# Kernel tuning notes

Measured on AMD Instinct MI355X. Metric: run time of the kernel, lower is better.

The kernel has to match this reference:

```python
import jax, jax.numpy as jnp
import numpy as np

B, C, L = 8192, 1, 4096
SCALES = 5
OUT_DIM = 512
STD_FACTOR = 1.0
SQRT_HALF = 0.7071067811865476  # Haar filter coefficient 1/sqrt(2)


def setup_inputs() -> dict:
    key = jax.random.key(0)
    k1, k2 = jax.random.split(key)
    x = jax.random.normal(k1, (B, C, L), dtype=jnp.float32)
    # kaiming_uniform_(a=0): bound = sqrt(2) * sqrt(3 / fan_in)
    fan_in = L  # in_dim_wave == in_dim for dyadic Haar
    bound = np.sqrt(2.0) * np.sqrt(3.0 / fan_in)
    block_mat = jax.random.uniform(k2, (L, OUT_DIM), dtype=jnp.float32,
                                   minval=-bound, maxval=bound)
    return {"x": x, "block_mat": block_mat}


def haar_analysis(x, scales):
    """Multi-level Haar DWT over last axis. Returns [cA_n, cD_n, ..., cD_1]."""
    details = []
    cur = x
    for _ in range(scales):
        even, odd = cur[..., ::2], cur[..., 1::2]
        details.append((even - odd) * SQRT_HALF)  # highpass
        cur = (even + odd) * SQRT_HALF            # lowpass
    return [cur] + details[::-1]


def reference(x, block_mat):
    coeffs = haar_analysis(x, SCALES)
    x_freq_cat = jnp.concatenate(coeffs, axis=-1)        # [B, C, L]
    c_no = x_freq_cat.shape[-1]
    x_freq_mat = x_freq_cat.reshape(-1, c_no)            # [B*C, L]
    a = jnp.abs(x_freq_mat)
    # torch.std is unbiased (ddof=1)
    threshold = jnp.mean(a) + jnp.std(a, ddof=1) * STD_FACTOR
    mask = a > threshold
    # sparse.mm(sparse(masked x), W) == (x * mask) @ W
    x_sparse = jnp.where(mask, x_freq_mat, jnp.zeros((), x_freq_mat.dtype))
    out = jax.nn.relu(x_sparse @ block_mat)              # [B*C, OUT_DIM]
    return out.reshape(x_freq_cat.shape[:-1] + (OUT_DIM,))
```

## Files before the change

kernel.cpp:

```cpp
#include <hip/hip_runtime.h>
#include <hip/hip_bf16.h>
#include <math.h>

#define LDIM 4096
#define NROWS 8192
#define NOUT 512

static const float SQRT_HALF_F = 0.70710678118654752440f;

typedef __attribute__((ext_vector_type(8))) short short8;
typedef __attribute__((ext_vector_type(4))) float f32x4;
typedef __attribute__((ext_vector_type(8))) unsigned short u16x8;
typedef __attribute__((ext_vector_type(4))) unsigned short u16x4;
typedef __attribute__((ext_vector_type(2))) unsigned short u16x2;

#define AM_OFF   0ull
#define WT_OFF   67108864ull
#define PART_OFF (WT_OFF + 4194304ull)
#define THR_OFF  (PART_OFF + 131072ull)

__device__ inline unsigned short f2bf(float f) {
  union { float f; unsigned u; } v; v.f = f;
  unsigned r = (v.u + 0x7fffu + ((v.u >> 16) & 1u)) >> 16;
  return (unsigned short)r;
}

__device__ inline unsigned short mcvt(float f, float thr) {
  return f2bf((fabsf(f) > thr) ? f : 0.0f);
}

__device__ inline void async16(void* l, const void* g) {
  __builtin_amdgcn_global_load_lds((const __attribute__((address_space(1))) void*)g,
                                   (__attribute__((address_space(3))) void*)l, 16, 0, 0);
}

__global__ __launch_bounds__(256) void haar1_kernel(const float* __restrict__ x,
                                                    double* __restrict__ partials,
                                                    const float* __restrict__ W,
                                                    unsigned short* __restrict__ Wt) {
  if (blockIdx.x >= NROWS) {
    __shared__ float tile[32][33];
    const int wb = blockIdx.x - NROWS;
    const int bx = wb & 15;
    const int by = wb >> 4;
    const int tx = threadIdx.x & 31, ty = threadIdx.x >> 5;
#pragma unroll
    for (int j = 0; j < 4; ++j)
      tile[ty + j * 8][tx] = W[(size_t)(by * 32 + ty + j * 8) * NOUT + bx * 32 + tx];
    __syncthreads();
#pragma unroll
    for (int j = 0; j < 4; ++j)
      Wt[(size_t)(bx * 32 + ty + j * 8) * LDIM + by * 32 + tx] = f2bf(tile[tx][ty + j * 8]);
    return;
  }

  __shared__ double red[8];
  const int row = blockIdx.x;
  const int t = threadIdx.x;
  const float S = SQRT_HALF_F;

  const float4* xr = (const float4*)(x + (size_t)row * LDIM) + 4 * t;
  float v[16];
#pragma unroll
  for (int k = 0; k < 4; ++k) {
    float4 q = xr[k];
    v[4 * k] = q.x; v[4 * k + 1] = q.y; v[4 * k + 2] = q.z; v[4 * k + 3] = q.w;
  }

  double sa = 0.0, sq = 0.0;
  float a1[8], a2[4], a3[2], a4;
#pragma unroll
  for (int j = 0; j < 8; ++j) {
    float d = (v[2 * j] - v[2 * j + 1]) * S;
    a1[j] = (v[2 * j] + v[2 * j + 1]) * S;
    sa += (double)fabsf(d); sq += (double)d * (double)d;
  }
#pragma unroll
  for (int j = 0; j < 4; ++j) {
    float d = (a1[2 * j] - a1[2 * j + 1]) * S;
    a2[j] = (a1[2 * j] + a1[2 * j + 1]) * S;
    sa += (double)fabsf(d); sq += (double)d * (double)d;
  }
#pragma unroll
  for (int j = 0; j < 2; ++j) {
    float d = (a2[2 * j] - a2[2 * j + 1]) * S;
    a3[j] = (a2[2 * j] + a2[2 * j + 1]) * S;
    sa += (double)fabsf(d); sq += (double)d * (double)d;
  }
  {
    float d = (a3[0] - a3[1]) * S;
    a4 = (a3[0] + a3[1]) * S;
    sa += (double)fabsf(d); sq += (double)d * (double)d;
  }
  {
    float other = __shfl_xor(a4, 1, 64);
    if ((t & 1) == 0) {
      float d = (a4 - other) * S, ap = (a4 + other) * S;
      sa += (double)fabsf(d) + (double)fabsf(ap);
      sq += (double)d * (double)d + (double)ap * (double)ap;
    }
  }

  const int lane = t & 63, wid = t >> 6;
#pragma unroll
  for (int off = 32; off > 0; off >>= 1) {
    sa += __shfl_down(sa, off, 64);
    sq += __shfl_down(sq, off, 64);
  }
  if (lane == 0) { red[wid] = sa; red[4 + wid] = sq; }
  __syncthreads();
  if (t == 0) {
    partials[2 * (size_t)row + 0] = red[0] + red[1] + red[2] + red[3];
    partials[2 * (size_t)row + 1] = red[4] + red[5] + red[6] + red[7];
  }
}

__global__ __launch_bounds__(1024) void thr_kernel(const double* __restrict__ partials,
                                                   float* __restrict__ thr) {
  __shared__ double red[32];
  const int tid = threadIdx.x;
  double sa = 0.0, sq = 0.0;
#pragma unroll
  for (int k = 0; k < NROWS / 1024; ++k) {
    int i = tid + k * 1024;
    sa += partials[2 * i + 0];
    sq += partials[2 * i + 1];
  }
  const int lane = tid & 63, wid = tid >> 6;
#pragma unroll
  for (int off = 32; off > 0; off >>= 1) {
    sa += __shfl_down(sa, off, 64);
    sq += __shfl_down(sq, off, 64);
  }
  if (lane == 0) { red[wid] = sa; red[16 + wid] = sq; }
  __syncthreads();
  if (tid == 0) {
    double s = 0.0, q = 0.0;
#pragma unroll
    for (int i = 0; i < 16; ++i) { s += red[i]; q += red[16 + i]; }
    const double n = (double)NROWS * (double)LDIM;
    double mean = s / n;
    double var = (q - s * s / n) / (n - 1.0);
    *thr = (float)(mean + sqrt(var));
  }
}

__global__ __launch_bounds__(256) void haar2_kernel(const float* __restrict__ x,
                                                    const float* __restrict__ thrp,
                                                    unsigned short* __restrict__ Am) {
  const float thr = *thrp;
  const int row = blockIdx.x;
  const int t = threadIdx.x;
  const float S = SQRT_HALF_F;

  const float4* xr = (const float4*)(x + (size_t)row * LDIM) + 4 * t;
  float v[16];
#pragma unroll
  for (int k = 0; k < 4; ++k) {
    float4 q = xr[k];
    v[4 * k] = q.x; v[4 * k + 1] = q.y; v[4 * k + 2] = q.z; v[4 * k + 3] = q.w;
  }

  unsigned short* orow = Am + (size_t)row * LDIM;
  float a1[8], a2[4], a3[2], a4;

  u16x8 d1;
#pragma unroll
  for (int j = 0; j < 8; ++j) {
    float d = (v[2 * j] - v[2 * j + 1]) * S;
    a1[j] = (v[2 * j] + v[2 * j + 1]) * S;
    d1[j] = mcvt(d, thr);
  }
  *(u16x8*)(orow + 2048 + 8 * t) = d1;

  u16x4 d2;
#pragma unroll
  for (int j = 0; j < 4; ++j) {
    float d = (a1[2 * j] - a1[2 * j + 1]) * S;
    a2[j] = (a1[2 * j] + a1[2 * j + 1]) * S;
    d2[j] = mcvt(d, thr);
  }
  *(u16x4*)(orow + 1024 + 4 * t) = d2;

  u16x2 d3;
#pragma unroll
  for (int j = 0; j < 2; ++j) {
    float d = (a2[2 * j] - a2[2 * j + 1]) * S;
    a3[j] = (a2[2 * j] + a2[2 * j + 1]) * S;
    d3[j] = mcvt(d, thr);
  }
  *(u16x2*)(orow + 512 + 2 * t) = d3;

  {
    float d = (a3[0] - a3[1]) * S;
    a4 = (a3[0] + a3[1]) * S;
    orow[256 + t] = mcvt(d, thr);
  }
  {
    float other = __shfl_xor(a4, 1, 64);
    if ((t & 1) == 0) {
      float d = (a4 - other) * S, ap = (a4 + other) * S;
      orow[128 + t / 2] = mcvt(d, thr);
      orow[t / 2] = mcvt(ap, thr);
    }
  }
}

__global__ __launch_bounds__(512) void gemm_kernel(const unsigned short* __restrict__ Am,
                                                   const unsigned short* __restrict__ Wt,
                                                   float* __restrict__ out) {
  __shared__ __align__(16) unsigned short As[128 * 64];
  __shared__ __align__(16) unsigned short Bs[64 * 64];

  const int tid = threadIdx.x;
  const int lane = tid & 63, w = tid >> 6;
  const int quad = lane >> 4, l15 = lane & 15;
  const int wm = w >> 1, wn = w & 1;

  const int id = blockIdx.x;
  const int xcd = id & 7, slot = id >> 3;
  const int nblk = slot & 7;
  const int mblk = (slot >> 3) * 8 + xcd;
  const int n0 = nblk * 64, m0 = mblk * 128;

  f32x4 acc[2][2] = {};

  const int rl = lane >> 3;
  const int cg = (lane & 7) ^ rl;
  const unsigned short* AgBase = Am + (size_t)(m0 + rl) * LDIM + cg * 8;
  const unsigned short* BgBase = Wt + (size_t)(n0 + rl) * LDIM + cg * 8;

  for (int k0 = 0; k0 < LDIM; k0 += 64) {
#pragma unroll
    for (int j = 0; j < 2; ++j)
      async16(&As[(w * 2 + j) * 512], AgBase + (size_t)((w * 2 + j) * 8) * LDIM + k0);
    async16(&Bs[w * 512], BgBase + (size_t)(w * 8) * LDIM + k0);
    __syncthreads();

    short8 af[2][2], bf[2][2];
#pragma unroll
    for (int mi = 0; mi < 2; ++mi) {
      const int row = wm * 32 + mi * 16 + l15;
#pragma unroll
      for (int ks = 0; ks < 2; ++ks)
        af[mi][ks] = *(const short8*)&As[row * 64 + ((ks * 4 + quad) ^ (row & 7)) * 8];
    }
#pragma unroll
    for (int ni = 0; ni < 2; ++ni) {
      const int row = wn * 32 + ni * 16 + l15;
#pragma unroll
      for (int ks = 0; ks < 2; ++ks)
        bf[ni][ks] = *(const short8*)&Bs[row * 64 + ((ks * 4 + quad) ^ (row & 7)) * 8];
    }
#pragma unroll
    for (int ks = 0; ks < 2; ++ks)
#pragma unroll
      for (int mi = 0; mi < 2; ++mi)
#pragma unroll
        for (int ni = 0; ni < 2; ++ni)
          acc[mi][ni] = __builtin_amdgcn_mfma_f32_16x16x32_bf16(af[mi][ks], bf[ni][ks],
                                                                acc[mi][ni], 0, 0, 0);
    __syncthreads();
  }

#pragma unroll
  for (int mi = 0; mi < 2; ++mi) {
#pragma unroll
    for (int ni = 0; ni < 2; ++ni) {
      const int r0 = m0 + wm * 32 + mi * 16 + quad * 4;
      const int c = n0 + wn * 32 + ni * 16 + l15;
#pragma unroll
      for (int r = 0; r < 4; ++r)
        out[(size_t)(r0 + r) * NOUT + c] = fmaxf(acc[mi][ni][r], 0.0f);
    }
  }
}

extern "C" void kernel_launch(void* const* d_in, const int* in_sizes, int n_in,
                              void* d_out, int out_size, void* d_ws, size_t ws_size,
                              hipStream_t stream) {
  const float* x = (const float*)d_in[0];
  const float* W = (const float*)d_in[1];
  float* out = (float*)d_out;

  char* ws = (char*)d_ws;
  unsigned short* Am = (unsigned short*)(ws + AM_OFF);
  unsigned short* Wt = (unsigned short*)(ws + WT_OFF);
  double* partials = (double*)(ws + PART_OFF);
  float* thr = (float*)(ws + THR_OFF);

  haar1_kernel<<<NROWS + 2048, 256, 0, stream>>>(x, partials, W, Wt);
  thr_kernel<<<1, 1024, 0, stream>>>(partials, thr);
  haar2_kernel<<<NROWS, 256, 0, stream>>>(x, thr, Am);
  gemm_kernel<<<512, 512, 0, stream>>>(Am, Wt, out);
}
```

Measured before the change: 268.0 us.

## Restructure GEMM as intra-block split-K with per-wave double-buffered async loads

The GEMM now uses 64x64 output tiles with 256-thread blocks, where each of the four waves owns a separate quarter of the K dimension. Each wave stages its slices into private LDS double buffers via async loads, waiting on vmcnt instead of block-wide barriers. The per-wave partial sums are reduced through LDS at the end, then ReLU is applied and stores are vectorized. This removes per-iteration __syncthreads and overlaps loads with MFMA, at the cost of extra LDS reduction traffic and lower tile reuse from the smaller M tile.

Result: slower. 286.5 us (+6.9%).

```diff
diff --git a/kernel.cpp b/kernel.cpp
--- a/kernel.cpp
+++ b/kernel.cpp
@@ -206,73 +206,99 @@
   }
 }
 
-__global__ __launch_bounds__(512) void gemm_kernel(const unsigned short* __restrict__ Am,
-                                                   const unsigned short* __restrict__ Wt,
-                                                   float* __restrict__ out) {
-  __shared__ __align__(16) unsigned short As[128 * 64];
-  __shared__ __align__(16) unsigned short Bs[64 * 64];
+__global__ __launch_bounds__(256, 2) void gemm_kernel(const unsigned short* __restrict__ Am,
+                                                      const unsigned short* __restrict__ Wt,
+                                                      float* __restrict__ out) {
+  __shared__ __align__(16) unsigned short lds[4 * 2 * 4096];
 
   const int tid = threadIdx.x;
   const int lane = tid & 63, w = tid >> 6;
   const int quad = lane >> 4, l15 = lane & 15;
-  const int wm = w >> 1, wn = w & 1;
 
   const int id = blockIdx.x;
   const int xcd = id & 7, slot = id >> 3;
   const int nblk = slot & 7;
   const int mblk = (slot >> 3) * 8 + xcd;
-  const int n0 = nblk * 64, m0 = mblk * 128;
-
-  f32x4 acc[2][2] = {};
-
-  const int rl = lane >> 3;
-  const int cg = (lane & 7) ^ rl;
-  const unsigned short* AgBase = Am + (size_t)(m0 + rl) * LDIM + cg * 8;
-  const unsigned short* BgBase = Wt + (size_t)(n0 + rl) * LDIM + cg * 8;
-
-  for (int k0 = 0; k0 < LDIM; k0 += 64) {
-#pragma unroll
-    for (int j = 0; j < 2; ++j)
-      async16(&As[(w * 2 + j) * 512], AgBase + (size_t)((w * 2 + j) * 8) * LDIM + k0);
-    async16(&Bs[w * 512], BgBase + (size_t)(w * 8) * LDIM + k0);
-    __syncthreads();
-
-    short8 af[2][2], bf[2][2];
-#pragma unroll
-    for (int mi = 0; mi < 2; ++mi) {
-      const int row = wm * 32 + mi * 16 + l15;
-#pragma unroll
-      for (int ks = 0; ks < 2; ++ks)
-        af[mi][ks] = *(const short8*)&As[row * 64 + ((ks * 4 + quad) ^ (row & 7)) * 8];
-    }
-#pragma unroll
-    for (int ni = 0; ni < 2; ++ni) {
-      const int row = wn * 32 + ni * 16 + l15;
-#pragma unroll
-      for (int ks = 0; ks < 2; ++ks)
-        bf[ni][ks] = *(const short8*)&Bs[row * 64 + ((ks * 4 + quad) ^ (row & 7)) * 8];
-    }
-#pragma unroll
-    for (int ks = 0; ks < 2; ++ks)
-#pragma unroll
-      for (int mi = 0; mi < 2; ++mi)
-#pragma unroll
-        for (int ni = 0; ni < 2; ++ni)
-          acc[mi][ni] = __builtin_amdgcn_mfma_f32_16x16x32_bf16(af[mi][ks], bf[ni][ks],
-                                                                acc[mi][ni], 0, 0, 0);
-    __syncthreads();
-  }
-
-#pragma unroll
-  for (int mi = 0; mi < 2; ++mi) {
-#pragma unroll
-    for (int ni = 0; ni < 2; ++ni) {
-      const int r0 = m0 + wm * 32 + mi * 16 + quad * 4;
-      const int c = n0 + wn * 32 + ni * 16 + l15;
-#pragma unroll
-      for (int r = 0; r < 4; ++r)
-        out[(size_t)(r0 + r) * NOUT + c] = fmaxf(acc[mi][ni][r], 0.0f);
-    }
+  const int n0 = nblk * 64, m0 = mblk * 64;
+
+  f32x4 acc[4][4] = {};
+
+  const int r = lane >> 2, p = lane & 3;
+  const int c = p ^ ((r >> 1) & 3);
+  const int kw = w * 32;
+  const unsigned short* Ag = Am + (size_t)(m0 + r) * LDIM + kw + c * 8;
+  const unsigned short* Bg = Wt + (size_t)(n0 + r) * LDIM + kw + c * 8;
+
+  unsigned short* wbase = &lds[w * 8192];
+
+  const int sw = (quad ^ ((l15 >> 1) & 3)) * 8;
+
+#define GEMM_ISSUE(T, B)                                                        \
+  {                                                                             \
+    const size_t ko = (size_t)(T) * 128;                                        \
+    unsigned short* Ad_ = wbase + (B) * 4096;                                   \
+    unsigned short* Bd_ = Ad_ + 2048;                                           \
+    _Pragma("unroll")                                                           \
+    for (int g = 0; g < 4; ++g) {                                               \
+      async16(Ad_ + g * 512, Ag + (size_t)(g * 16) * LDIM + ko);                \
+      async16(Bd_ + g * 512, Bg + (size_t)(g * 16) * LDIM + ko);                \
+    }                                                                           \
+  }
+
+#define GEMM_COMPUTE(B)                                                         \
+  {                                                                             \
+    const unsigned short* Ad_ = wbase + (B) * 4096;                             \
+    const unsigned short* Bd_ = Ad_ + 2048;                                     \
+    short8 af[4], bf[4];                                                        \
+    _Pragma("unroll")                                                           \
+    for (int mi = 0; mi < 4; ++mi)                                              \
+      af[mi] = *(const short8*)&Ad_[mi * 512 + l15 * 32 + sw];                  \
+    _Pragma("unroll")                                                           \
+    for (int ni = 0; ni < 4; ++ni)                                              \
+      bf[ni] = *(const short8*)&Bd_[ni * 512 + l15 * 32 + sw];                  \
+    _Pragma("unroll")                                                           \
+    for (int mi = 0; mi < 4; ++mi)                                              \
+      _Pragma("unroll")                                                         \
+      for (int ni = 0; ni < 4; ++ni)                                            \
+        acc[mi][ni] = __builtin_amdgcn_mfma_f32_16x16x32_bf16(af[mi], bf[ni],   \
+                                                              acc[mi][ni], 0, 0, 0); \
+  }
+
+  GEMM_ISSUE(0, 0);
+  for (int t = 0; t < 31; ++t) {
+    GEMM_ISSUE(t + 1, (t + 1) & 1);
+    asm volatile("s_waitcnt vmcnt(8)" ::: "memory");
+    GEMM_COMPUTE(t & 1);
+  }
+  asm volatile("s_waitcnt vmcnt(0)" ::: "memory");
+  GEMM_COMPUTE(1);
+
+#undef GEMM_ISSUE
+#undef GEMM_COMPUTE
+
+  __syncthreads();
+  float* fl = (float*)lds;
+#pragma unroll
+  for (int mi = 0; mi < 4; ++mi)
+#pragma unroll
+    for (int ni = 0; ni < 4; ++ni)
+#pragma unroll
+      for (int rr = 0; rr < 4; ++rr)
+        fl[w * 4096 + (mi * 16 + quad * 4 + rr) * 64 + ni * 16 + l15] = acc[mi][ni][rr];
+  __syncthreads();
+
+  const int orow = tid >> 2, ocb = (tid & 3) * 16;
+  const size_t obase = (size_t)(m0 + orow) * NOUT + n0 + ocb;
+#pragma unroll
+  for (int j = 0; j < 4; ++j) {
+    const int off = orow * 64 + ocb + j * 4;
+    f32x4 s = *(const f32x4*)&fl[off];
+#pragma unroll
+    for (int ww = 1; ww < 4; ++ww) s += *(const f32x4*)&fl[ww * 4096 + off];
+    f32x4 rlu;
+#pragma unroll
+    for (int k = 0; k < 4; ++k) rlu[k] = fmaxf(s[k], 0.0f);
+    *(f32x4*)&out[obase + j * 4] = rlu;
   }
 }
 
@@ -292,5 +318,5 @@
   haar1_kernel<<<NROWS + 2048, 256, 0, stream>>>(x, partials, W, Wt);
   thr_kernel<<<1, 1024, 0, stream>>>(partials, thr);
   haar2_kernel<<<NROWS, 256, 0, stream>>>(x, thr, Am);
-  gemm_kernel<<<512, 512, 0, stream>>>(Am, Wt, out);
-}
+  gemm_kernel<<<1024, 256, 0, stream>>>(Am, Wt, out);
+}
```
